# Kernel optimization log

Measured on AMD Instinct MI355X. Metric: run time of the kernel, lower is better.

## Reference

```python
import jax, jax.numpy as jnp
import numpy as np

B, S, D = 2, 2048, 768
H, HD = 12, 64            # num_heads, head_dim
TOPO = 128                # topology_dim
NH, HB = 8, 64            # num_hashes, hash_bits
TEMP = 0.1                # lsh_temperature
SCALE = float(np.sqrt(HD))
LSH_THRESH = 0.3
NEG = -10000.0


def setup_inputs() -> dict:
    key = jax.random.key(0)
    ks = jax.random.split(key, 12)
    hidden_states = jax.random.normal(ks[0], (B, S, D), jnp.float32)
    topo_features = jax.random.normal(ks[1], (B, S, TOPO), jnp.float32)
    attention_mask = jnp.ones((B, S), jnp.int32)
    s = 0.02
    Wq = jax.random.normal(ks[2], (D, D), jnp.float32) * s
    Wk = jax.random.normal(ks[3], (D, D), jnp.float32) * s
    Wv = jax.random.normal(ks[4], (D, D), jnp.float32) * s
    Wo = jax.random.normal(ks[5], (D, D), jnp.float32) * s
    bo = jnp.zeros((D,), jnp.float32)
    Wg = jax.random.normal(ks[6], (D + TOPO, D), jnp.float32) * s
    bg = jnp.zeros((D,), jnp.float32)
    hash_proj = jax.random.normal(ks[7], (NH, D, HB), jnp.float32) * 0.02
    topology_bias = jnp.zeros((NH, HB), jnp.float32)
    return {
        "hidden_states": hidden_states, "topo_features": topo_features,
        "Wq": Wq, "Wk": Wk, "Wv": Wv, "Wo": Wo, "bo": bo,
        "Wg": Wg, "bg": bg, "hash_proj": hash_proj,
        "topology_bias": topology_bias, "attention_mask": attention_mask,
    }


def reference(hidden_states, topo_features, Wq, Wk, Wv, Wo, bo, Wg, bg,
              hash_proj, topology_bias, attention_mask):
    hs, tf = hidden_states, topo_features
    # QKV projections -> [B,H,S,HD]
    q = (hs @ Wq).reshape(B, S, H, HD).transpose(0, 2, 1, 3)
    k = (hs @ Wk).reshape(B, S, H, HD).transpose(0, 2, 1, 3)
    v = (hs @ Wv).reshape(B, S, H, HD).transpose(0, 2, 1, 3)
    scores = jnp.einsum('bhqd,bhkd->bhqk', q, k) / SCALE  # [B,H,S,S]

    # LSH hash codes (queries == keys == hidden_states)
    proj = jnp.einsum('bsd,hdk->bshk', hs, hash_proj)
    proj = proj + TEMP * jnp.einsum('bsd,hdk->bshk', tf, hash_proj[:, :TOPO, :])
    proj = proj + topology_bias[None, None]  # [B,S,NH,HB]
    codes = jnp.sign(proj)
    # hash similarity averaged over hash tables -> [B,S,S]
    sim = jnp.einsum('bqhc,bkhc->bhqk', codes, codes) / HB
    sim = sim.mean(axis=1)
    lsh_keep = sim > LSH_THRESH
    scores = jnp.where(lsh_keep[:, None], scores, NEG)

    pad_keep = (attention_mask != 0)[:, None, None, :]  # [B,1,1,S]
    scores = jnp.where(pad_keep, scores, NEG)

    probs = jax.nn.softmax(scores, axis=-1)
    context = jnp.einsum('bhqk,bhkd->bqhd', probs, v).reshape(B, S, D)

    gate = jax.nn.sigmoid(jnp.concatenate([context, tf], axis=-1) @ Wg + bg)
    context = gate * context + (1.0 - gate) * hs
    return context @ Wo + bo
```

## Files before the change

### kernel.cpp

```cpp
#include <hip/hip_runtime.h>

typedef __attribute__((ext_vector_type(4))) float v4f;
typedef __attribute__((ext_vector_type(8))) short v8s;

#define BB 2
#define SS 2048
#define DD 768
#define HH 12
#define HDIM 64
#define NWORDS 8
#define HAM_MAX 179

#define OFF_QBF    ((size_t)0)
#define OFF_HSBF   ((size_t)31457280)
#define OFF_TFBF   ((size_t)37748736)
#define OFF_CTXBF  ((size_t)38797312)
#define OFF_CTX2BF ((size_t)45088768)
#define OFF_WTQKV  ((size_t)51380224)
#define OFF_WGT    ((size_t)54919168)
#define OFF_WOT    ((size_t)56295424)
#define OFF_HPWT   ((size_t)57475072)
#define OFF_CODES  ((size_t)66781184)
#define OFF_KEEP   ((size_t)67043328)
#define OFF_CMASK  ((size_t)68091904)

__device__ inline short f2bf(float x) {
    unsigned u = __float_as_uint(x);
    u = (u + 0x7FFFu + ((u >> 16) & 1u)) >> 16;
    return (short)u;
}
__device__ inline float bf2f(short s) {
    return __uint_as_float(((unsigned)(unsigned short)s) << 16);
}

__device__ __forceinline__ void load_lds16(const void* g, void* l) {
    __builtin_amdgcn_global_load_lds((const __attribute__((address_space(1))) void*)g,
                                     (__attribute__((address_space(3))) void*)l,
                                     16, 0, 0);
}

__global__ __launch_bounds__(256) void prep(
    const float* __restrict__ hs, const float* __restrict__ tf,
    const float* __restrict__ Wq, const float* __restrict__ Wk,
    const float* __restrict__ Wv, const float* __restrict__ Wg,
    const float* __restrict__ Wo, const float* __restrict__ hp,
    short* __restrict__ hsbf, short* __restrict__ tfbf,
    short* __restrict__ wtqkv, short* __restrict__ wgT,
    short* __restrict__ woT, short* __restrict__ hpwT,
    unsigned int* __restrict__ cmask) {
    __shared__ float T[32][33];
    const int blk = blockIdx.x;
    const int tid = threadIdx.x;
    if (blk < 1792) {
        if (blk == 0 && tid < 64) cmask[tid] = 0u;
        int i = blk * 256 + tid;
        const int na8 = 3145728 / 8;
        const float* src; short* dst; int off;
        if (i < na8) { src = hs; dst = hsbf; off = i << 3; }
        else         { src = tf; dst = tfbf; off = (i - na8) << 3; }
        float4 x = *(const float4*)(src + off);
        float4 y = *(const float4*)(src + off + 4);
        v8s r;
        r[0] = f2bf(x.x); r[1] = f2bf(x.y); r[2] = f2bf(x.z); r[3] = f2bf(x.w);
        r[4] = f2bf(y.x); r[5] = f2bf(y.y); r[6] = f2bf(y.z); r[7] = f2bf(y.w);
        *(v8s*)(dst + off) = r;
        return;
    }
    const int tx = tid & 31, ty = tid >> 5;
    if (blk < 3520) {
        int b = blk - 1792;
        int z = b / 576, rem = b % 576;
        int x = rem % 24, y = rem / 24;
        const float* W = (z == 0) ? Wq : (z == 1) ? Wk : Wv;
        short* Wt = wtqkv + (size_t)z * 589824;
        int n0 = x * 32, k0 = y * 32;
#pragma unroll
        for (int p = 0; p < 4; ++p) {
            int kk = ty + p * 8;
            T[tx][kk] = W[(size_t)(k0 + kk) * 768 + n0 + tx];
        }
        __syncthreads();
#pragma unroll
        for (int p = 0; p < 4; ++p) {
            int nn = ty + p * 8;
            Wt[(size_t)(n0 + nn) * 768 + k0 + tx] = f2bf(T[nn][tx]);
        }
    } else if (blk < 4192) {
        int b = blk - 3520;
        int x = b % 24, y = b / 24;
        int n0 = x * 32, k0 = y * 32;
#pragma unroll
        for (int p = 0; p < 4; ++p) {
            int kk = ty + p * 8;
            T[tx][kk] = Wg[(size_t)(k0 + kk) * 768 + n0 + tx];
        }
        __syncthreads();
#pragma unroll
        for (int p = 0; p < 4; ++p) {
            int nn = ty + p * 8;
            wgT[(size_t)(n0 + nn) * 896 + k0 + tx] = f2bf(T[nn][tx]);
        }
    } else if (blk < 4768) {
        int b = blk - 4192;
        int x = b % 24, y = b / 24;
        int n0 = x * 32, k0 = y * 32;
#pragma unroll
        for (int p = 0; p < 4; ++p) {
            int kk = ty + p * 8;
            T[tx][kk] = Wo[(size_t)(k0 + kk) * 768 + n0 + tx];
        }
        __syncthreads();
#pragma unroll
        for (int p = 0; p < 4; ++p) {
            int nn = ty + p * 8;
            woT[(size_t)(n0 + nn) * 768 + k0 + tx] = f2bf(T[nn][tx]);
        }
    } else {
        int b = blk - 4768;
        int x = b % 28, y = b / 28;
        int kk0 = x * 32, hc0 = y * 32;
        int h = hc0 >> 6, cb = hc0 & 63;
#pragma unroll
        for (int p = 0; p < 4; ++p) {
            int kp = ty + p * 8;
            int gk = kk0 + kp;
            int ks = (gk >= 768) ? gk - 768 : gk;
            float f = hp[((size_t)h * 768 + ks) * 64 + cb + tx];
            T[tx][kp] = (gk >= 768) ? 0.1f * f : f;
        }
        __syncthreads();
#pragma unroll
        for (int p = 0; p < 4; ++p) {
            int cp = ty + p * 8;
            hpwT[(size_t)(hc0 + cp) * 896 + kk0 + tx] = f2bf(T[cp][tx]);
        }
    }
}

template<int WN, int NW, int MF>
__global__ __launch_bounds__(256) void gemm_mfma(
    const short* __restrict__ A, const short* __restrict__ A2,
    const short* __restrict__ Bt, const short* __restrict__ Bt2,
    const float* __restrict__ bias,
    float* __restrict__ outF, short* __restrict__ outB,
    unsigned long long* __restrict__ codesOut,
    int N, int K1, int K2, int mode,
    const short* __restrict__ gctxb, const short* __restrict__ ghsb) {
    constexpr int BN = WN * 32;
    constexpr int BM = MF * 32;
    __shared__ __align__(16) short As[2 * BM * 64];
    __shared__ __align__(16) short Bs[2 * NW * BN * 64];
    const int t = threadIdx.x;
    const int lane = t & 63, wave = t >> 6;
    const int wm = wave >> 1, wn = wave & 1;
    const int l15 = lane & 15, l4 = lane >> 4;

    const int nbx = gridDim.x;
    const int perXcd = gridDim.y >> 3;
    int flat = blockIdx.x + nbx * blockIdx.y;
    int xcd = flat & 7, j = flat >> 3;
    int by = xcd * perXcd + j / nbx;
    int bx = j % nbx;
    const int row0 = by * BM;

    int nWact, col0, myMode, Kblk;
    const short* Bp;
    const float* biasp = bias;
    if (mode == 3) {
        if (bx < 12) { nWact = NW; col0 = bx * 64;         myMode = 1; Kblk = K1;      Bp = Bt;  biasp = nullptr; }
        else         { nWact = 2;  col0 = (bx - 12) * 128; myMode = 0; Kblk = K1 + K2; Bp = Bt2; }
    } else {
        nWact = 1; col0 = bx * BN; myMode = mode; Kblk = K1 + K2; Bp = Bt;
    }
    const bool sepW = (myMode == 1);

    const int lrow = lane >> 3;
    const int scolS = ((lane & 7) ^ lrow) << 3;

    auto STAGE = [&](int buf, int k0) {
        const short* Ap; int ks, strideS;
        if (k0 < K1) { Ap = A;  ks = k0;      strideS = K1; }
        else         { Ap = A2; ks = k0 - K1; strideS = K2; }
#pragma unroll
        for (int qq = 0; qq < MF; ++qq) {
            int c = wave * MF + qq;
            const short* ga = Ap + (size_t)(row0 + c * 8 + lrow) * strideS + ks + scolS;
            load_lds16(ga, (char*)As + buf * (BM * 128) + c * 1024);
        }
#pragma unroll
        for (int w = 0; w < NW; ++w) {
            if (w < nWact) {
#pragma unroll
                for (int qq = 0; qq < WN; ++qq) {
                    int c = wave * WN + qq;
                    size_t rowIdx = (size_t)(col0 + (sepW ? 0 : w * 64) + c * 8 + lrow);
                    const short* gb = Bp + (sepW ? (size_t)w * 589824 : (size_t)0) +
                                      rowIdx * Kblk + k0 + scolS;
                    load_lds16(gb, (char*)Bs + (buf * NW + w) * (BN * 128) + c * 1024);
                }
            }
        }
    };

    v4f acc[NW][MF][WN];
#pragma unroll
    for (int w = 0; w < NW; ++w)
#pragma unroll
        for (int m = 0; m < MF; ++m)
#pragma unroll
            for (int n = 0; n < WN; ++n) acc[w][m][n] = (v4f){0.f, 0.f, 0.f, 0.f};

    const int nK = Kblk >> 6;
    STAGE(0, 0);
    __syncthreads();
    int cur = 0;
    for (int kt = 0; kt < nK; ++kt) {
        if (kt + 1 < nK) STAGE(cur ^ 1, (kt + 1) << 6);
#pragma unroll
        for (int kk = 0; kk < 2; ++kk) {
            v8s a[MF];
#pragma unroll
            for (int m = 0; m < MF; ++m) {
                int row = wm * (MF * 16) + m * 16 + l15;
                int byte = (row * 128 + kk * 64 + l4 * 16) ^ ((row & 7) << 4);
                a[m] = *(const v8s*)((const char*)As + cur * (BM * 128) + byte);
            }
#pragma unroll
            for (int w = 0; w < NW; ++w) {
                if (w < nWact) {
                    v8s b[WN];
#pragma unroll
                    for (int n = 0; n < WN; ++n) {
                        int row = wn * (WN * 16) + n * 16 + l15;
                        int byte = (row * 128 + kk * 64 + l4 * 16) ^ ((row & 7) << 4);
                        b[n] = *(const v8s*)((const char*)Bs + (cur * NW + w) * (BN * 128) + byte);
                    }
#pragma unroll
                    for (int m = 0; m < MF; ++m)
#pragma unroll
                        for (int n = 0; n < WN; ++n)
                            acc[w][m][n] = __builtin_amdgcn_mfma_f32_16x16x32_bf16(a[m], b[n], acc[w][m][n], 0, 0, 0);
                }
            }
        }
        __syncthreads();
        cur ^= 1;
    }

    if (mode == 3 && myMode == 0) {
        unsigned short* pieces = (unsigned short*)As;
#pragma unroll
        for (int w = 0; w < 2; ++w)
#pragma unroll
            for (int m = 0; m < MF; ++m)
#pragma unroll
                for (int n = 0; n < WN; ++n) {
                    int gc = col0 + w * 64 + (wn * WN + n) * 16 + l15;
                    int part = w * 4 + wn * WN + n;
#pragma unroll
                    for (int i = 0; i < 4; ++i) {
                        float c = acc[w][m][n][i] + biasp[gc];
                        unsigned long long bal = __ballot(c > 0.f);
                        if (lane < 4) {
                            int rloc = wm * (MF * 16) + m * 16 + lane * 4 + i;
                            pieces[rloc * 8 + part] = (unsigned short)(bal >> (lane * 16));
                        }
                    }
                }
        __syncthreads();
        if (t < 256) {
            int row = t >> 1, word = t & 1;
            const unsigned short* pp = pieces + row * 8 + word * 4;
            unsigned long long w64 = (unsigned long long)pp[0]
                | ((unsigned long long)pp[1] << 16)
                | ((unsigned long long)pp[2] << 32)
                | ((unsigned long long)pp[3] << 48);
            codesOut[(size_t)(row0 + row) * NWORDS + ((col0 >> 6) + word)] = w64;
        }
        return;
    }

    if (myMode == 1) {
        short* stg = (short*)As;
        const int hh = col0 >> 6;
        const int bb = row0 >> 11;
        const int s0 = row0 & 2047;
#pragma unroll
        for (int w = 0; w < NW; ++w) {
            if (w < nWact) {
                __syncthreads();
#pragma unroll
                for (int m = 0; m < MF; ++m)
#pragma unroll
                    for (int n = 0; n < WN; ++n) {
                        int r = wm * (MF * 16) + m * 16 + l4 * 4;
                        int c = (wn * WN + n) * 16 + l15;
#pragma unroll
                        for (int i = 0; i < 4; ++i)
                            stg[(r + i) * 64 + c] = f2bf(acc[w][m][n][i]);
                    }
                __syncthreads();
                short* dst = outB + (size_t)w * 3145728 +
                             (((size_t)(bb * HH + hh)) * SS + s0) * HDIM;
                const char* src = (const char*)stg + t * (BM / 2);
                char* d = (char*)dst + t * (BM / 2);
#pragma unroll
                for (int q = 0; q < BM / 32; ++q)
                    *(int4*)(d + q * 16) = *(const int4*)(src + q * 16);
            }
        }
        return;
    }

#pragma unroll
    for (int m = 0; m < MF; ++m) {
#pragma unroll
        for (int n = 0; n < WN; ++n) {
            int gr0 = row0 + (wm * MF + m) * 16 + l4 * 4;
            int gc = col0 + (wn * WN + n) * 16 + l15;
#pragma unroll
            for (int i = 0; i < 4; ++i) {
                int gr = gr0 + i;
                if (myMode == 0) {
                    float c = acc[0][m][n][i];
                    if (biasp) c += biasp[gc];
                    outF[(size_t)gr * N + gc] = c;
                } else {
                    float c = acc[0][m][n][i] + biasp[gc];
                    float g = 1.f / (1.f + __expf(-c));
                    size_t off = (size_t)gr * N + gc;
                    float cv = bf2f(gctxb[off]);
                    float hv = bf2f(ghsb[off]);
                    outB[off] = f2bf(g * cv + (1.f - g) * hv);
                }
            }
        }
    }
}

__global__ __launch_bounds__(256) void mask_kernel(
    const unsigned long long* __restrict__ codes, const int* __restrict__ mask,
    unsigned long long* __restrict__ keepArr, unsigned int* __restrict__ chunkmask) {
    __shared__ unsigned long long ckS[64][NWORDS];
    __shared__ int mskS[64];
    const int t = threadIdx.x;
    const int r = t >> 2, tx = t & 3;
    const int qc = blockIdx.x, kc = blockIdx.y, b = blockIdx.z;
    const int q0 = qc << 6, k0 = kc << 6;

#pragma unroll
    for (int p = 0; p < 2; ++p) {
        int idx = t + (p << 8);
        int jr = idx >> 3, ww = idx & 7;
        ckS[jr][ww ^ (jr >> 4)] =
            codes[((size_t)(b * SS + k0 + jr)) * NWORDS + ww];
    }
    if (t < 64) mskS[t] = mask[b * SS + k0 + t];
    unsigned long long cq[NWORDS];
    {
        const unsigned long long* cp = codes + ((size_t)(b * SS + q0 + r)) * NWORDS;
#pragma unroll
        for (int w = 0; w < NWORDS; ++w) cq[w] = cp[w];
    }
    __syncthreads();

    unsigned long long k64 = 0;
#pragma unroll
    for (int j16 = 0; j16 < 16; ++j16) {
        int j = (tx << 4) + j16;
        int ham = 0;
#pragma unroll
        for (int w = 0; w < NWORDS; ++w)
            ham += __popcll(cq[w] ^ ckS[j][w ^ tx]);
        if (ham <= HAM_MAX && mskS[j]) k64 |= 1ull << j;
    }
    k64 |= __shfl_xor(k64, 1, 4);
    k64 |= __shfl_xor(k64, 2, 4);
    if (tx == 0) keepArr[((size_t)(b * SS + q0 + r)) * 32 + kc] = k64;
    if (__syncthreads_or(k64 != 0) && t == 0)
        atomicOr(&chunkmask[b * 32 + qc], 1u << kc);
}

__global__ __launch_bounds__(256) void attn_kernel(
    const short* __restrict__ qm, const short* __restrict__ km,
    const short* __restrict__ vm, const unsigned long long* __restrict__ keepArr,
    const unsigned int* __restrict__ chunkmask, short* __restrict__ ctxbf) {
    __shared__ __align__(16) short Qs[64][72];
    __shared__ __align__(16) short Ks[64][72];
    __shared__ __align__(16) short VT[64][72];
    __shared__ __align__(16) short Ps[64][72];
    __shared__ unsigned long long keepS[64];
    const int t = threadIdx.x;
    const int lane = t & 63, wave = t >> 6;
    const int l15 = lane & 15, l4 = lane >> 4;
    const int q0 = blockIdx.x << 6;
    const int bh = blockIdx.y;
    const int b = bh / HH, h = bh % HH;

    {
        int r = t >> 2, seg = t & 3;
        const short* g = qm + ((size_t)bh * SS + q0 + r) * HDIM + seg * 16;
        *(int4*)&Qs[r][seg * 16] = *(const int4*)g;
        *(int4*)&Qs[r][seg * 16 + 8] = *(const int4*)(g + 8);
    }
    unsigned int cm = chunkmask[b * 32 + blockIdx.x];
    float mrun[4], lrun[4];
    v4f oacc[4];
#pragma unroll
    for (int i = 0; i < 4; ++i) { mrun[i] = -1e30f; lrun[i] = 0.f; }
#pragma unroll
    for (int n = 0; n < 4; ++n) oacc[n] = (v4f){0.f, 0.f, 0.f, 0.f};

    while (cm) {
        int kc = __ffs(cm) - 1;
        cm &= cm - 1;
        __syncthreads();
        if (t < 64) keepS[t] = keepArr[((size_t)(b * SS + q0 + t)) * 32 + kc];
        {
            int key = t >> 2, seg = t & 3;
            const short* gk = km + ((size_t)bh * SS + (kc << 6) + key) * HDIM + seg * 16;
            *(int4*)&Ks[key][seg * 16] = *(const int4*)gk;
            *(int4*)&Ks[key][seg * 16 + 8] = *(const int4*)(gk + 8);
            const short* gv = vm + ((size_t)bh * SS + (kc << 6) + key) * HDIM + seg * 16;
            int4 v0 = *(const int4*)gv, v1 = *(const int4*)(gv + 8);
            const short* s0 = (const short*)&v0;
            const short* s1 = (const short*)&v1;
#pragma unroll
            for (int e = 0; e < 8; ++e) VT[seg * 16 + e][key] = s0[e];
#pragma unroll
            for (int e = 0; e < 8; ++e) VT[seg * 16 + 8 + e][key] = s1[e];
        }
        __syncthreads();

        v8s qa0 = *(const v8s*)&Qs[wave * 16 + l15][l4 * 8];
        v8s qa1 = *(const v8s*)&Qs[wave * 16 + l15][32 + l4 * 8];
        v4f sacc[4];
#pragma unroll
        for (int n = 0; n < 4; ++n) sacc[n] = (v4f){0.f, 0.f, 0.f, 0.f};
#pragma unroll
        for (int n = 0; n < 4; ++n) {
            v8s kb0 = *(const v8s*)&Ks[n * 16 + l15][l4 * 8];
            v8s kb1 = *(const v8s*)&Ks[n * 16 + l15][32 + l4 * 8];
            sacc[n] = __builtin_amdgcn_mfma_f32_16x16x32_bf16(qa0, kb0, sacc[n], 0, 0, 0);
            sacc[n] = __builtin_amdgcn_mfma_f32_16x16x32_bf16(qa1, kb1, sacc[n], 0, 0, 0);
        }
        unsigned long long kp[4];
#pragma unroll
        for (int i = 0; i < 4; ++i) kp[i] = keepS[wave * 16 + l4 * 4 + i];
        float pe[4][4], mloc[4];
#pragma unroll
        for (int i = 0; i < 4; ++i) mloc[i] = -1e30f;
#pragma unroll
        for (int n = 0; n < 4; ++n)
#pragma unroll
            for (int i = 0; i < 4; ++i) {
                bool keep = (kp[i] >> (n * 16 + l15)) & 1;
                float sv = keep ? sacc[n][i] * 0.125f : -1e30f;
                pe[n][i] = sv;
                mloc[i] = fmaxf(mloc[i], sv);
            }
#pragma unroll
        for (int i = 0; i < 4; ++i) {
            mloc[i] = fmaxf(mloc[i], __shfl_xor(mloc[i], 1, 16));
            mloc[i] = fmaxf(mloc[i], __shfl_xor(mloc[i], 2, 16));
            mloc[i] = fmaxf(mloc[i], __shfl_xor(mloc[i], 4, 16));
            mloc[i] = fmaxf(mloc[i], __shfl_xor(mloc[i], 8, 16));
        }
        float psum[4] = {0.f, 0.f, 0.f, 0.f};
#pragma unroll
        for (int n = 0; n < 4; ++n)
#pragma unroll
            for (int i = 0; i < 4; ++i) {
                bool keep = pe[n][i] > -1e29f;
                float mnew = fmaxf(mrun[i], mloc[i]);
                float p = keep ? __expf(pe[n][i] - mnew) : 0.f;
                pe[n][i] = p;
                psum[i] += p;
            }
#pragma unroll
        for (int i = 0; i < 4; ++i) {
            psum[i] += __shfl_xor(psum[i], 1, 16);
            psum[i] += __shfl_xor(psum[i], 2, 16);
            psum[i] += __shfl_xor(psum[i], 4, 16);
            psum[i] += __shfl_xor(psum[i], 8, 16);
            float mnew = fmaxf(mrun[i], mloc[i]);
            float scale = __expf(mrun[i] - mnew);
            lrun[i] = lrun[i] * scale + psum[i];
            mrun[i] = mnew;
#pragma unroll
            for (int n = 0; n < 4; ++n) oacc[n][i] *= scale;
        }
#pragma unroll
        for (int n = 0; n < 4; ++n)
#pragma unroll
            for (int i = 0; i < 4; ++i)
                Ps[wave * 16 + l4 * 4 + i][n * 16 + l15] = f2bf(pe[n][i]);
        __syncthreads();

        v8s pa0 = *(const v8s*)&Ps[wave * 16 + l15][l4 * 8];
        v8s pa1 = *(const v8s*)&Ps[wave * 16 + l15][32 + l4 * 8];
#pragma unroll
        for (int n = 0; n < 4; ++n) {
            v8s vb0 = *(const v8s*)&VT[n * 16 + l15][l4 * 8];
            v8s vb1 = *(const v8s*)&VT[n * 16 + l15][32 + l4 * 8];
            oacc[n] = __builtin_amdgcn_mfma_f32_16x16x32_bf16(pa0, vb0, oacc[n], 0, 0, 0);
            oacc[n] = __builtin_amdgcn_mfma_f32_16x16x32_bf16(pa1, vb1, oacc[n], 0, 0, 0);
        }
    }
    float invl[4];
#pragma unroll
    for (int i = 0; i < 4; ++i) invl[i] = lrun[i] > 0.f ? 1.f / lrun[i] : 0.f;
#pragma unroll
    for (int n = 0; n < 4; ++n)
#pragma unroll
        for (int i = 0; i < 4; ++i) {
            int r = wave * 16 + l4 * 4 + i;
            size_t off = ((size_t)b * SS + q0 + r) * DD + h * HDIM + n * 16 + l15;
            ctxbf[off] = f2bf(oacc[n][i] * invl[i]);
        }
}

extern "C" void kernel_launch(void* const* d_in, const int* in_sizes, int n_in,
                              void* d_out, int out_size, void* d_ws, size_t ws_size,
                              hipStream_t stream) {
    const float* hs = (const float*)d_in[0];
    const float* tf = (const float*)d_in[1];
    const float* Wq = (const float*)d_in[2];
    const float* Wk = (const float*)d_in[3];
    const float* Wv = (const float*)d_in[4];
    const float* Wo = (const float*)d_in[5];
    const float* bo = (const float*)d_in[6];
    const float* Wg = (const float*)d_in[7];
    const float* bg = (const float*)d_in[8];
    const float* hp = (const float*)d_in[9];
    const float* tb = (const float*)d_in[10];
    const int* msk  = (const int*)d_in[11];
    float* out = (float*)d_out;

    char* w = (char*)d_ws;
    short* qkvbf  = (short*)(w + OFF_QBF);
    short* hsbf   = (short*)(w + OFF_HSBF);
    short* tfbf   = (short*)(w + OFF_TFBF);
    short* ctxbf  = (short*)(w + OFF_CTXBF);
    short* ctx2bf = (short*)(w + OFF_CTX2BF);
    short* wtqkv  = (short*)(w + OFF_WTQKV);
    short* wgT    = (short*)(w + OFF_WGT);
    short* woT    = (short*)(w + OFF_WOT);
    short* hpwT   = (short*)(w + OFF_HPWT);
    unsigned long long* codes = (unsigned long long*)(w + OFF_CODES);
    unsigned long long* keepA = (unsigned long long*)(w + OFF_KEEP);
    unsigned int* cmask = (unsigned int*)(w + OFF_CMASK);

    prep<<<dim3(5216), 256, 0, stream>>>(
        hs, tf, Wq, Wk, Wv, Wg, Wo, hp,
        hsbf, tfbf, wtqkv, wgT, woT, hpwT, cmask);
    gemm_mfma<2, 3, 4><<<dim3(16, 32), 256, 0, stream>>>(
        hsbf, tfbf, wtqkv, hpwT, tb, nullptr, qkvbf, codes,
        512, 768, 128, 3, nullptr, nullptr);
    mask_kernel<<<dim3(32, 32, 2), 256, 0, stream>>>(codes, msk, keepA, cmask);
    attn_kernel<<<dim3(32, 24), 256, 0, stream>>>(
        qkvbf, qkvbf + 3145728, qkvbf + 2 * 3145728, keepA, cmask, ctxbf);
    gemm_mfma<2, 1, 2><<<dim3(12, 64), 256, 0, stream>>>(
        ctxbf, tfbf, wgT, nullptr, bg, nullptr, ctx2bf, nullptr,
        768, 768, 128, 2, ctxbf, hsbf);
    gemm_mfma<2, 1, 2><<<dim3(12, 64), 256, 0, stream>>>(
        ctx2bf, nullptr, woT, nullptr, bo, out, nullptr, nullptr,
        768, 768, 0, 0, nullptr, nullptr);
}
```

Baseline: 94.45 us.

## Exploit Hamming symmetry in mask kernel and raise MFMA wave priority

The mask kernel now computes only upper-triangular (qc<=kc) chunk pairs and writes the transposed keep bits for the mirrored block, since Hamming distance is symmetric. This roughly halves the popcount work and the launch count (528 blocks instead of 1024 per batch). Padding masks are gathered with a ballot per block rather than per-key shared loads. The attention kernel also wraps its MFMA sections in s_setprio to favour matrix issue. Each block now does a shared-memory transpose and two atomics, and the mask kernel is a small part of the total time.

```diff
diff --git a/kernel.cpp b/kernel.cpp
--- a/kernel.cpp
+++ b/kernel.cpp
@@ -342,10 +342,14 @@
     const unsigned long long* __restrict__ codes, const int* __restrict__ mask,
     unsigned long long* __restrict__ keepArr, unsigned int* __restrict__ chunkmask) {
     __shared__ unsigned long long ckS[64][NWORDS];
-    __shared__ int mskS[64];
+    __shared__ unsigned long long rowBits[64];
+    __shared__ unsigned long long maskW[2];
     const int t = threadIdx.x;
     const int r = t >> 2, tx = t & 3;
-    const int qc = blockIdx.x, kc = blockIdx.y, b = blockIdx.z;
+    int i = blockIdx.x, qc = 0;
+    while (i >= 32 - qc) { i -= 32 - qc; ++qc; }
+    const int kc = qc + i;
+    const int b = blockIdx.y;
     const int q0 = qc << 6, k0 = kc << 6;
 
 #pragma unroll
@@ -355,7 +359,13 @@
         ckS[jr][ww ^ (jr >> 4)] =
             codes[((size_t)(b * SS + k0 + jr)) * NWORDS + ww];
     }
-    if (t < 64) mskS[t] = mask[b * SS + k0 + t];
+    if (t < 64) {
+        unsigned long long bm = __ballot(mask[b * SS + k0 + (t & 63)] != 0);
+        if (t == 0) maskW[0] = bm;
+    } else if (t < 128) {
+        unsigned long long bm = __ballot(mask[b * SS + q0 + (t & 63)] != 0);
+        if ((t & 63) == 0) maskW[1] = bm;
+    }
     unsigned long long cq[NWORDS];
     {
         const unsigned long long* cp = codes + ((size_t)(b * SS + q0 + r)) * NWORDS;
@@ -364,7 +374,7 @@
     }
     __syncthreads();
 
-    unsigned long long k64 = 0;
+    unsigned long long kham = 0;
 #pragma unroll
     for (int j16 = 0; j16 < 16; ++j16) {
         int j = (tx << 4) + j16;
@@ -372,13 +382,35 @@
 #pragma unroll
         for (int w = 0; w < NWORDS; ++w)
             ham += __popcll(cq[w] ^ ckS[j][w ^ tx]);
-        if (ham <= HAM_MAX && mskS[j]) k64 |= 1ull << j;
-    }
-    k64 |= __shfl_xor(k64, 1, 4);
-    k64 |= __shfl_xor(k64, 2, 4);
-    if (tx == 0) keepArr[((size_t)(b * SS + q0 + r)) * 32 + kc] = k64;
-    if (__syncthreads_or(k64 != 0) && t == 0)
-        atomicOr(&chunkmask[b * 32 + qc], 1u << kc);
+        if (ham <= HAM_MAX) kham |= 1ull << j;
+    }
+    kham |= __shfl_xor(kham, 1, 4);
+    kham |= __shfl_xor(kham, 2, 4);
+    unsigned long long k64 = kham & maskW[0];
+    if (tx == 0) {
+        keepArr[((size_t)(b * SS + q0 + r)) * 32 + kc] = k64;
+        rowBits[r] = kham;
+    }
+    bool any1 = __syncthreads_or(k64 != 0);
+
+    unsigned long long t64 = 0;
+    if (kc != qc) {
+#pragma unroll
+        for (int qq = 0; qq < 16; ++qq) {
+            int q = (tx << 4) + qq;
+            t64 |= ((rowBits[q] >> r) & 1ull) << q;
+        }
+        t64 |= __shfl_xor(t64, 1, 4);
+        t64 |= __shfl_xor(t64, 2, 4);
+        t64 &= maskW[1];
+        if (tx == 0)
+            keepArr[((size_t)(b * SS + k0 + r)) * 32 + qc] = t64;
+    }
+    bool any2 = __syncthreads_or(t64 != 0);
+    if (t == 0) {
+        if (any1) atomicOr(&chunkmask[b * 32 + qc], 1u << kc);
+        if (any2) atomicOr(&chunkmask[b * 32 + kc], 1u << qc);
+    }
 }
 
 __global__ __launch_bounds__(256) void attn_kernel(
@@ -437,6 +469,7 @@
         v4f sacc[4];
 #pragma unroll
         for (int n = 0; n < 4; ++n) sacc[n] = (v4f){0.f, 0.f, 0.f, 0.f};
+        __builtin_amdgcn_s_setprio(1);
 #pragma unroll
         for (int n = 0; n < 4; ++n) {
             v8s kb0 = *(const v8s*)&Ks[n * 16 + l15][l4 * 8];
@@ -444,6 +477,7 @@
             sacc[n] = __builtin_amdgcn_mfma_f32_16x16x32_bf16(qa0, kb0, sacc[n], 0, 0, 0);
             sacc[n] = __builtin_amdgcn_mfma_f32_16x16x32_bf16(qa1, kb1, sacc[n], 0, 0, 0);
         }
+        __builtin_amdgcn_s_setprio(0);
         unsigned long long kp[4];
 #pragma unroll
         for (int i = 0; i < 4; ++i) kp[i] = keepS[wave * 16 + l4 * 4 + i];
@@ -499,6 +533,7 @@
 
         v8s pa0 = *(const v8s*)&Ps[wave * 16 + l15][l4 * 8];
         v8s pa1 = *(const v8s*)&Ps[wave * 16 + l15][32 + l4 * 8];
+        __builtin_amdgcn_s_setprio(1);
 #pragma unroll
         for (int n = 0; n < 4; ++n) {
             v8s vb0 = *(const v8s*)&VT[n * 16 + l15][l4 * 8];
@@ -506,6 +541,7 @@
             oacc[n] = __builtin_amdgcn_mfma_f32_16x16x32_bf16(pa0, vb0, oacc[n], 0, 0, 0);
             oacc[n] = __builtin_amdgcn_mfma_f32_16x16x32_bf16(pa1, vb1, oacc[n], 0, 0, 0);
         }
+        __builtin_amdgcn_s_setprio(0);
     }
     float invl[4];
 #pragma unroll
@@ -557,7 +593,7 @@
     gemm_mfma<2, 3, 4><<<dim3(16, 32), 256, 0, stream>>>(
         hsbf, tfbf, wtqkv, hpwT, tb, nullptr, qkvbf, codes,
         512, 768, 128, 3, nullptr, nullptr);
-    mask_kernel<<<dim3(32, 32, 2), 256, 0, stream>>>(codes, msk, keepA, cmask);
+    mask_kernel<<<dim3(528, 2), 256, 0, stream>>>(codes, msk, keepA, cmask);
     attn_kernel<<<dim3(32, 24), 256, 0, stream>>>(
         qkvbf, qkvbf + 3145728, qkvbf + 2 * 3145728, keepA, cmask, ctxbf);
     gemm_mfma<2, 1, 2><<<dim3(12, 64), 256, 0, stream>>>(
```

After: 93.48 us. Within noise of the previous version (-1.0%).
